# Kernel optimization log

Hardware: AMD Instinct MI355X
Metric: run time of the kernel (lower is better)

Reference implementation:

```python
import jax, jax.numpy as jnp
import numpy as np

N, E = 100000, 1600000
F_IN, H, C = 64, 64, 40


def setup_inputs() -> dict:
    key = jax.random.key(0)
    k = jax.random.split(key, 6)
    x = jax.random.normal(k[0], (N, F_IN), jnp.float32)
    edge_index = jax.random.randint(k[1], (2, E), 0, N, jnp.int32)
    edge_weight = jax.random.uniform(k[2], (E,), jnp.float32)
    W1 = jax.random.normal(k[3], (F_IN, H), jnp.float32) / np.sqrt(F_IN)
    b1 = jnp.zeros((H,), jnp.float32)
    W2 = jax.random.normal(k[4], (H, C), jnp.float32) / np.sqrt(H)
    b2 = jnp.zeros((C,), jnp.float32)
    return {"x": x, "edge_index": edge_index, "edge_weight": edge_weight,
            "W1": W1, "b1": b1, "W2": W2, "b2": b2}


def reference(x, edge_index, edge_weight, W1, b1, W2, b2):
    # PyG GCNConv: add self-loops (weight 1), symmetric normalization
    # D^{-1/2} (A + I) D^{-1/2}, linear transform, scatter-add, bias.
    n = x.shape[0]
    src, dst = edge_index[0], edge_index[1]
    loop = jnp.arange(n, dtype=src.dtype)
    src_f = jnp.concatenate([src, loop])
    dst_f = jnp.concatenate([dst, loop])
    w_f = jnp.concatenate([edge_weight, jnp.ones((n,), edge_weight.dtype)])
    deg = jax.ops.segment_sum(w_f, dst_f, num_segments=n)
    dinv = jnp.where(deg > 0, jax.lax.rsqrt(deg), 0.0)
    norm = dinv[src_f] * w_f * dinv[dst_f]  # [E+N]

    def conv(h, W, b):
        h = h @ W                                    # [n, d_out]
        msg = h[src_f] * norm[:, None]               # gather + scale, [E+N, d_out]
        return jax.ops.segment_sum(msg, dst_f, num_segments=n) + b

    h = jax.nn.relu(conv(x, W1, b1))
    # dropout is identity in eval mode (training=False)
    h = conv(h, W2, b2)
    return jax.nn.log_softmax(h, axis=1)
```

## Files before the change

kernel.cpp:

```cpp
#include <hip/hip_runtime.h>
#include <math.h>

#define N_NODES 100000
#define N_EDGES 1600000
#define C_DIM 40
#define NGROUPS 6250

#define BSZ 256
#define NB  ((N_NODES + BSZ - 1) / BSZ)
#define EB  4096
#define NBE ((N_EDGES + EB - 1) / EB)

#define OFF_DINV 0
#define OFF_BB   100000
#define OFF_CS   100392
#define OFF_ROW  100800
#define OFF_H    200802
#define OFF_REC2 353684
#define OFF_H1P  3553684
#define OFF_H2P  6753684
#define OFF_AGG1 9953684

typedef float floatx4 __attribute__((ext_vector_type(4)));
typedef short shortx8 __attribute__((ext_vector_type(8)));

__device__ inline unsigned short f2bf(float f) {
    unsigned int u = __float_as_uint(f);
    u += 0x7FFF + ((u >> 16) & 1);
    return (unsigned short)(u >> 16);
}
__device__ inline float bf2f(unsigned short h) {
    return __uint_as_float(((unsigned int)h) << 16);
}
__device__ inline float bflo(unsigned int u) { return __uint_as_float(u << 16); }
__device__ inline float bfhi(unsigned int u) { return __uint_as_float(u & 0xFFFF0000u); }

__global__ __launch_bounds__(512) void k_hist2d(const int* __restrict__ ei,
                                                int* __restrict__ H,
                                                int* __restrict__ colsum) {
    __shared__ int bins[NB];
    int t = threadIdx.x, b = blockIdx.x;
    for (int i = t; i < NB; i += 512) bins[i] = 0;
    __syncthreads();
    int base = b * EB;
    for (int i = t; i < EB; i += 512) {
        int e = base + i;
        if (e < N_EDGES) atomicAdd(&bins[ei[N_EDGES + e] >> 8], 1);
    }
    __syncthreads();
    for (int i = t; i < NB; i += 512) {
        int c = bins[i];
        H[b * NB + i] = c;
        if (c) atomicAdd(&colsum[i], c);
    }
}

__global__ __launch_bounds__(512) void k_colscan(int* __restrict__ H,
                                                 const int* __restrict__ colsum,
                                                 int* __restrict__ bucketBase,
                                                 int* __restrict__ rowStart) {
    __shared__ int sd[512];
    __shared__ int sbase;
    int t = threadIdx.x, j = blockIdx.x;
    int p = 0;
    for (int i = t; i < j; i += 512) p += colsum[i];
    sd[t] = p;
    __syncthreads();
    for (int off = 256; off > 0; off >>= 1) {
        if (t < off) sd[t] += sd[t + off];
        __syncthreads();
    }
    if (t == 0) sbase = sd[0];
    __syncthreads();
    int base = sbase;
    if (t == 0) {
        bucketBase[j] = base;
        if (j == NB - 1) { bucketBase[NB] = base + colsum[j]; rowStart[N_NODES] = N_EDGES; }
    }
    __syncthreads();
    int val = (t < NBE) ? H[t * NB + j] : 0;
    sd[t] = val;
    __syncthreads();
    for (int off = 1; off < 512; off <<= 1) {
        int v = (t >= off) ? sd[t - off] : 0;
        __syncthreads();
        sd[t] += v;
        __syncthreads();
    }
    if (t < NBE) H[t * NB + j] = base + sd[t] - val;
}

__global__ __launch_bounds__(512) void k_scatter(const int* __restrict__ ei,
                                                 const float* __restrict__ w,
                                                 const int* __restrict__ blockBase,
                                                 int2* __restrict__ rec) {
    __shared__ int bases[NB];
    __shared__ int cur[NB];
    int t = threadIdx.x, b = blockIdx.x;
    for (int i = t; i < NB; i += 512) { bases[i] = blockBase[b * NB + i]; cur[i] = 0; }
    __syncthreads();
    int base = b * EB;
    for (int i = t; i < EB; i += 512) {
        int e = base + i;
        if (e < N_EDGES) {
            int s = ei[e], d = ei[N_EDGES + e];
            float wv = w[e];
            int bin = d >> 8;
            int pos = bases[bin] + atomicAdd(&cur[bin], 1);
            rec[pos] = make_int2(s | ((d & 255) << 17), __float_as_int(wv));
        }
    }
}

__global__ __launch_bounds__(512) void k_bsort(const int* __restrict__ bucketBase,
                                               const int2* __restrict__ rec,
                                               int2* __restrict__ rec2,
                                               float* __restrict__ dinv,
                                               int* __restrict__ rowStart) {
    __shared__ int   cnt[256];
    __shared__ float wsum[256];
    __shared__ int   cur[256];
    __shared__ int   sd[512];
    int t = threadIdx.x, b = blockIdx.x;
    if (t < 256) { cnt[t] = 0; wsum[t] = 0.f; }
    __syncthreads();
    int r0 = bucketBase[b], r1 = bucketBase[b + 1];
    for (int i = r0 + t; i < r1; i += 512) {
        int2 rv = rec[i];
        int l = (rv.x >> 17) & 255;
        atomicAdd(&cnt[l], 1);
        atomicAdd(&wsum[l], __int_as_float(rv.y));
    }
    __syncthreads();
    int val = (t < 256) ? cnt[t] : 0;
    sd[t] = val;
    __syncthreads();
    for (int off = 1; off < 512; off <<= 1) {
        int v = (t >= off) ? sd[t - off] : 0;
        __syncthreads();
        sd[t] += v;
        __syncthreads();
    }
    float dloc = 0.f;
    if (t < 256) {
        int excl = sd[t] - val;
        cur[t] = excl;
        int node = b * BSZ + t;
        dloc = rsqrtf(1.f + wsum[t]);
        if (node < N_NODES) {
            rowStart[node] = r0 + excl;
            dinv[node] = dloc;
        }
    }
    __syncthreads();
    if (t < 256) wsum[t] = dloc;
    __syncthreads();
    for (int i = r0 + t; i < r1; i += 512) {
        int2 rv = rec[i];
        int l = (rv.x >> 17) & 255;
        float cpart = __int_as_float(rv.y) * wsum[l];
        int pos = r0 + atomicAdd(&cur[l], 1);
        rec2[pos] = make_int2((rv.x & 0x1FFFF) << 7, __float_as_int(cpart));
    }
}

__global__ __launch_bounds__(256) void k_mm1(const float* __restrict__ x,
                                             const float* __restrict__ W1,
                                             const float* __restrict__ dinv,
                                             unsigned short* __restrict__ h1p) {
    int t = threadIdx.x, lane = t & 63, wv = t >> 6;
    int m = lane & 15, quad = lane >> 4;
    int wid = blockIdx.x * 4 + wv, nw = gridDim.x * 4;
    shortx8 B[2][4];
#pragma unroll
    for (int kc = 0; kc < 2; ++kc)
#pragma unroll
        for (int tt = 0; tt < 4; ++tt)
#pragma unroll
            for (int j = 0; j < 8; ++j) {
                int k = kc * 32 + quad * 8 + j;
                B[kc][tt][j] = (short)f2bf(W1[k * 64 + tt * 16 + m]);
            }
    for (int g = wid; g < NGROUPS; g += nw) {
        int n0 = g * 16;
        const float* xr = x + (long)(n0 + m) * 64 + quad * 8;
        floatx4 xa = ((const floatx4*)xr)[0];
        floatx4 xb = ((const floatx4*)(xr + 4))[0];
        floatx4 xc = ((const floatx4*)(xr + 32))[0];
        floatx4 xd = ((const floatx4*)(xr + 36))[0];
        shortx8 A0, A1;
#pragma unroll
        for (int j = 0; j < 4; ++j) {
            A0[j] = (short)f2bf(xa[j]);
            A0[4 + j] = (short)f2bf(xb[j]);
            A1[j] = (short)f2bf(xc[j]);
            A1[4 + j] = (short)f2bf(xd[j]);
        }
        floatx4 acc[4];
#pragma unroll
        for (int tt = 0; tt < 4; ++tt) {
            acc[tt] = (floatx4){0.f, 0.f, 0.f, 0.f};
            acc[tt] = __builtin_amdgcn_mfma_f32_16x16x32_bf16(A0, B[0][tt], acc[tt], 0, 0, 0);
            acc[tt] = __builtin_amdgcn_mfma_f32_16x16x32_bf16(A1, B[1][tt], acc[tt], 0, 0, 0);
        }
        floatx4 dv = ((const floatx4*)(dinv + n0 + quad * 4))[0];
#pragma unroll
        for (int reg = 0; reg < 4; ++reg) {
            int node = n0 + quad * 4 + reg;
            float d = dv[reg];
#pragma unroll
            for (int tt = 0; tt < 4; ++tt)
                h1p[(long)node * 64 + tt * 16 + m] = f2bf(acc[tt][reg] * d);
        }
    }
}

__global__ __launch_bounds__(256) void k_agg1(const int* __restrict__ rowStart,
                                              const int2* __restrict__ rec2,
                                              const float* __restrict__ dinv,
                                              const unsigned short* __restrict__ h1p,
                                              float* __restrict__ agg1) {
    __shared__ int2 cache[4][64];
    int t = threadIdx.x, lane = t & 63, wv = t >> 6;
    int node = blockIdx.x * 4 + wv;
    if (node >= N_NODES) return;
    int2* wc = cache[wv];
    wc[lane] = make_int2(0, 0);
    const char* hb = (const char*)h1p;
    int eslot = lane >> 4;
    int c = lane & 15;
    int lo = c << 3;
    float dn = dinv[node];
    float a0 = 0.f, a1 = 0.f, a2 = 0.f, a3 = 0.f;
    float b0 = 0.f, b1 = 0.f, b2v = 0.f, b3 = 0.f;
    if (eslot == 0) {
        const unsigned int* sp = (const unsigned int*)(hb + ((long)node << 7) + lo);
        unsigned int u0 = sp[0], u1 = sp[1];
        a0 = bflo(u0) * dn; a1 = bfhi(u0) * dn;
        a2 = bflo(u1) * dn; a3 = bfhi(u1) * dn;
    }
    int s0 = rowStart[node], s1 = rowStart[node + 1];
    for (int base = s0; base < s1; base += 64) {
        int idx = base + lane;
        if (idx < s1) wc[lane] = rec2[idx];
        __builtin_amdgcn_wave_barrier();
        int cnt = min(64, s1 - base);
        int j = 0;
        for (; j + 7 < cnt; j += 8) {
            int2 eA = wc[j + eslot];
            int2 eB = wc[j + 4 + eslot];
            const unsigned int* pA = (const unsigned int*)(hb + eA.x + lo);
            const unsigned int* pB = (const unsigned int*)(hb + eB.x + lo);
            unsigned int uA0 = pA[0], uA1 = pA[1];
            unsigned int uB0 = pB[0], uB1 = pB[1];
            float cA = __int_as_float(eA.y), cB = __int_as_float(eB.y);
            a0 = fmaf(bflo(uA0), cA, a0);
            a1 = fmaf(bfhi(uA0), cA, a1);
            a2 = fmaf(bflo(uA1), cA, a2);
            a3 = fmaf(bfhi(uA1), cA, a3);
            b0 = fmaf(bflo(uB0), cB, b0);
            b1 = fmaf(bfhi(uB0), cB, b1);
            b2v = fmaf(bflo(uB1), cB, b2v);
            b3 = fmaf(bfhi(uB1), cB, b3);
        }
        for (; j < cnt; j += 4) {
            int jj = j + eslot;
            bool valid = jj < cnt;
            int2 e = wc[valid ? jj : j];
            float cc = valid ? __int_as_float(e.y) : 0.f;
            const unsigned int* p = (const unsigned int*)(hb + e.x + lo);
            unsigned int u0 = p[0], u1 = p[1];
            a0 = fmaf(bflo(u0), cc, a0);
            a1 = fmaf(bfhi(u0), cc, a1);
            a2 = fmaf(bflo(u1), cc, a2);
            a3 = fmaf(bfhi(u1), cc, a3);
        }
        __builtin_amdgcn_wave_barrier();
    }
    a0 += b0; a1 += b1; a2 += b2v; a3 += b3;
    a0 += __shfl_xor(a0, 16, 64); a0 += __shfl_xor(a0, 32, 64);
    a1 += __shfl_xor(a1, 16, 64); a1 += __shfl_xor(a1, 32, 64);
    a2 += __shfl_xor(a2, 16, 64); a2 += __shfl_xor(a2, 32, 64);
    a3 += __shfl_xor(a3, 16, 64); a3 += __shfl_xor(a3, 32, 64);
    if (eslot == 0) {
        *(float4*)(agg1 + ((long)node << 6) + (c << 2)) = make_float4(a0, a1, a2, a3);
    }
}

__global__ __launch_bounds__(256) void k_mm2(const float* __restrict__ agg1,
                                             const float* __restrict__ b1,
                                             const float* __restrict__ W2,
                                             const float* __restrict__ dinv,
                                             unsigned short* __restrict__ h2p) {
    int t = threadIdx.x, lane = t & 63, wv = t >> 6;
    int m = lane & 15, quad = lane >> 4;
    int wid = blockIdx.x * 4 + wv, nw = gridDim.x * 4;
    shortx8 B[2][3];
#pragma unroll
    for (int kc = 0; kc < 2; ++kc)
#pragma unroll
        for (int tt = 0; tt < 3; ++tt) {
            int n = tt * 16 + m;
#pragma unroll
            for (int j = 0; j < 8; ++j) {
                int k = kc * 32 + quad * 8 + j;
                B[kc][tt][j] = (n < C_DIM) ? (short)f2bf(W2[k * C_DIM + n]) : (short)0;
            }
        }
    floatx4 ba0 = ((const floatx4*)(b1 + quad * 8))[0];
    floatx4 ba1 = ((const floatx4*)(b1 + quad * 8 + 4))[0];
    floatx4 bb0 = ((const floatx4*)(b1 + 32 + quad * 8))[0];
    floatx4 bb1 = ((const floatx4*)(b1 + 32 + quad * 8 + 4))[0];
    for (int g = wid; g < NGROUPS; g += nw) {
        int n0 = g * 16;
        const float* xr = agg1 + (long)(n0 + m) * 64 + quad * 8;
        floatx4 xa = ((const floatx4*)xr)[0];
        floatx4 xb = ((const floatx4*)(xr + 4))[0];
        floatx4 xc = ((const floatx4*)(xr + 32))[0];
        floatx4 xd = ((const floatx4*)(xr + 36))[0];
        shortx8 A0, A1;
#pragma unroll
        for (int j = 0; j < 4; ++j) {
            A0[j]     = (short)f2bf(fmaxf(xa[j] + ba0[j], 0.f));
            A0[4 + j] = (short)f2bf(fmaxf(xb[j] + ba1[j], 0.f));
            A1[j]     = (short)f2bf(fmaxf(xc[j] + bb0[j], 0.f));
            A1[4 + j] = (short)f2bf(fmaxf(xd[j] + bb1[j], 0.f));
        }
        floatx4 acc[3];
#pragma unroll
        for (int tt = 0; tt < 3; ++tt) {
            acc[tt] = (floatx4){0.f, 0.f, 0.f, 0.f};
            acc[tt] = __builtin_amdgcn_mfma_f32_16x16x32_bf16(A0, B[0][tt], acc[tt], 0, 0, 0);
            acc[tt] = __builtin_amdgcn_mfma_f32_16x16x32_bf16(A1, B[1][tt], acc[tt], 0, 0, 0);
        }
        floatx4 dv = ((const floatx4*)(dinv + n0 + quad * 4))[0];
#pragma unroll
        for (int reg = 0; reg < 4; ++reg) {
            int node = n0 + quad * 4 + reg;
            float d = dv[reg];
#pragma unroll
            for (int tt = 0; tt < 3; ++tt) {
                int col = tt * 16 + m;
                if (col < C_DIM)
                    h2p[(long)node * 64 + col] = f2bf(acc[tt][reg] * d);
            }
        }
    }
}

__global__ __launch_bounds__(256) void k_agg2(const int* __restrict__ rowStart,
                                              const int2* __restrict__ rec2,
                                              const float* __restrict__ dinv,
                                              const unsigned short* __restrict__ h2p,
                                              const float* __restrict__ b2,
                                              float* __restrict__ out) {
    __shared__ int2 cache[4][64];
    int t = threadIdx.x, lane = t & 63, wv = t >> 6;
    int node = blockIdx.x * 4 + wv;
    if (node >= N_NODES) return;
    int2* wc = cache[wv];
    wc[lane] = make_int2(0, 0);
    const char* hb = (const char*)h2p;
    int eslot = lane / 20;
    int c = lane - eslot * 20;
    bool elane = eslot < 3;
    int lo = c << 2;
    float dn = dinv[node];
    float alo0 = 0.f, ahi0 = 0.f, alo1 = 0.f, ahi1 = 0.f;
    if (eslot == 0) {
        unsigned int u = *(const unsigned int*)(hb + ((long)node << 7) + lo);
        alo0 = bflo(u) * dn;
        ahi0 = bfhi(u) * dn;
    }
    int s0 = rowStart[node], s1 = rowStart[node + 1];
    for (int base = s0; base < s1; base += 64) {
        int idx = base + lane;
        if (idx < s1) wc[lane] = rec2[idx];
        __builtin_amdgcn_wave_barrier();
        int cnt = min(64, s1 - base);
        int j = 0;
        for (; j + 5 < cnt; j += 6) {
            int2 eA = wc[j + eslot];
            int2 eB = wc[j + 3 + eslot];
            unsigned int uA = *(const unsigned int*)(hb + eA.x + lo);
            unsigned int uB = *(const unsigned int*)(hb + eB.x + lo);
            float cA = elane ? __int_as_float(eA.y) : 0.f;
            float cB = elane ? __int_as_float(eB.y) : 0.f;
            alo0 = fmaf(bflo(uA), cA, alo0);
            ahi0 = fmaf(bfhi(uA), cA, ahi0);
            alo1 = fmaf(bflo(uB), cB, alo1);
            ahi1 = fmaf(bfhi(uB), cB, ahi1);
        }
        for (; j < cnt; j += 3) {
            int jj = j + eslot;
            bool valid = elane && (jj < cnt);
            int2 e = wc[valid ? jj : j];
            float cc = valid ? __int_as_float(e.y) : 0.f;
            unsigned int u = *(const unsigned int*)(hb + e.x + lo);
            alo0 = fmaf(bflo(u), cc, alo0);
            ahi0 = fmaf(bfhi(u), cc, ahi0);
        }
        __builtin_amdgcn_wave_barrier();
    }
    float alo = alo0 + alo1, ahi = ahi0 + ahi1;
    float t1 = __shfl(alo, lane + 20, 64), t2 = __shfl(alo, lane + 40, 64);
    float t3 = __shfl(ahi, lane + 20, 64), t4 = __shfl(ahi, lane + 40, 64);
    alo = alo + t1 + t2;
    ahi = ahi + t3 + t4;
    bool act = lane < 20;
    float2 bb = ((const float2*)b2)[c];
    float vlo = act ? alo + bb.x : -INFINITY;
    float vhi = act ? ahi + bb.y : -INFINITY;
    float m = fmaxf(vlo, vhi);
#pragma unroll
    for (int off = 32; off; off >>= 1) m = fmaxf(m, __shfl_xor(m, off, 64));
    float exlo = act ? expf(vlo - m) : 0.f;
    float exhi = act ? expf(vhi - m) : 0.f;
    float s = exlo + exhi;
#pragma unroll
    for (int off = 32; off; off >>= 1) s += __shfl_xor(s, off, 64);
    float ls = m + logf(s);
    if (act) {
        *(float2*)(out + (long)node * C_DIM + (c << 1)) = make_float2(vlo - ls, vhi - ls);
    }
}

extern "C" void kernel_launch(void* const* d_in, const int* in_sizes, int n_in,
                              void* d_out, int out_size, void* d_ws, size_t ws_size,
                              hipStream_t stream) {
    const float* x  = (const float*)d_in[0];
    const int*   ei = (const int*)d_in[1];
    const float* w  = (const float*)d_in[2];
    const float* W1 = (const float*)d_in[3];
    const float* b1 = (const float*)d_in[4];
    const float* W2 = (const float*)d_in[5];
    const float* b2 = (const float*)d_in[6];
    float* out = (float*)d_out;

    float* wsf = (float*)d_ws;
    int*   wsi = (int*)d_ws;
    float* dinv       = wsf + OFF_DINV;
    int*   bucketBase = wsi + OFF_BB;
    int*   colsum     = wsi + OFF_CS;
    int*   rowStart   = wsi + OFF_ROW;
    int*   H          = wsi + OFF_H;
    int2*  rec2       = (int2*)(wsi + OFF_REC2);
    int2*  rec        = (int2*)(wsi + OFF_H1P);
    unsigned short* h1p = (unsigned short*)(wsi + OFF_H1P);
    unsigned short* h2p = (unsigned short*)(wsi + OFF_H2P);
    float* agg1       = wsf + OFF_AGG1;

    hipMemsetAsync(colsum, 0, NB * sizeof(int), stream);
    k_hist2d<<<NBE, 512, 0, stream>>>(ei, H, colsum);
    k_colscan<<<NB, 512, 0, stream>>>(H, colsum, bucketBase, rowStart);
    k_scatter<<<NBE, 512, 0, stream>>>(ei, w, H, rec);
    k_bsort<<<NB, 512, 0, stream>>>(bucketBase, rec, rec2, dinv, rowStart);

    k_mm1<<<512, 256, 0, stream>>>(x, W1, dinv, h1p);
    k_agg1<<<(N_NODES + 3) / 4, 256, 0, stream>>>(rowStart, rec2, dinv, h1p, agg1);

    k_mm2<<<512, 256, 0, stream>>>(agg1, b1, W2, dinv, h2p);
    k_agg2<<<(N_NODES + 3) / 4, 256, 0, stream>>>(rowStart, rec2, dinv, h2p, b2, out);
}
```

Before: 279.5 us.

## Widen gather loads in aggregation kernels and fuse bias+ReLU+bf16 into agg1

The aggregation kernels now have each lane load 16-byte (agg1) or 8-byte (agg2) chunks of a neighbor row, so more edges are processed per wave iteration with fewer, wider gather instructions. agg1 also applies bias, ReLU and bf16 conversion before writing, so the intermediate is stored as a 64-wide bf16 array instead of fp32. This halves the intermediate traffic between agg1 and mm2 and moves the elementwise work out of mm2. Wider per-lane loads use more registers and spread fewer lanes across each row, which may change occupancy and coalescing.

```diff
diff --git a/kernel.cpp b/kernel.cpp
--- a/kernel.cpp
+++ b/kernel.cpp
@@ -19,7 +19,7 @@
 #define OFF_REC2 353684
 #define OFF_H1P  3553684
 #define OFF_H2P  6753684
-#define OFF_AGG1 9953684
+#define OFF_R1P  9953684
 
 typedef float floatx4 __attribute__((ext_vector_type(4)));
 typedef short shortx8 __attribute__((ext_vector_type(8)));
@@ -219,7 +219,8 @@
                                               const int2* __restrict__ rec2,
                                               const float* __restrict__ dinv,
                                               const unsigned short* __restrict__ h1p,
-                                              float* __restrict__ agg1) {
+                                              const float* __restrict__ b1,
+                                              unsigned short* __restrict__ r1p) {
     __shared__ int2 cache[4][64];
     int t = threadIdx.x, lane = t & 63, wv = t >> 6;
     int node = blockIdx.x * 4 + wv;
@@ -227,17 +228,18 @@
     int2* wc = cache[wv];
     wc[lane] = make_int2(0, 0);
     const char* hb = (const char*)h1p;
-    int eslot = lane >> 4;
-    int c = lane & 15;
-    int lo = c << 3;
+    int eslot = lane >> 3;
+    int c = lane & 7;
+    int lo = c << 4;
     float dn = dinv[node];
-    float a0 = 0.f, a1 = 0.f, a2 = 0.f, a3 = 0.f;
-    float b0 = 0.f, b1 = 0.f, b2v = 0.f, b3 = 0.f;
+    float a0 = 0, a1 = 0, a2 = 0, a3 = 0, a4 = 0, a5 = 0, a6 = 0, a7 = 0;
+    float g0 = 0, g1 = 0, g2 = 0, g3 = 0, g4 = 0, g5 = 0, g6 = 0, g7 = 0;
     if (eslot == 0) {
-        const unsigned int* sp = (const unsigned int*)(hb + ((long)node << 7) + lo);
-        unsigned int u0 = sp[0], u1 = sp[1];
-        a0 = bflo(u0) * dn; a1 = bfhi(u0) * dn;
-        a2 = bflo(u1) * dn; a3 = bfhi(u1) * dn;
+        uint4 u = *(const uint4*)(hb + ((long)node << 7) + lo);
+        a0 = bflo(u.x) * dn; a1 = bfhi(u.x) * dn;
+        a2 = bflo(u.y) * dn; a3 = bfhi(u.y) * dn;
+        a4 = bflo(u.z) * dn; a5 = bfhi(u.z) * dn;
+        a6 = bflo(u.w) * dn; a7 = bfhi(u.w) * dn;
     }
     int s0 = rowStart[node], s1 = rowStart[node + 1];
     for (int base = s0; base < s1; base += 64) {
@@ -246,49 +248,56 @@
         __builtin_amdgcn_wave_barrier();
         int cnt = min(64, s1 - base);
         int j = 0;
-        for (; j + 7 < cnt; j += 8) {
+        for (; j + 15 < cnt; j += 16) {
             int2 eA = wc[j + eslot];
-            int2 eB = wc[j + 4 + eslot];
-            const unsigned int* pA = (const unsigned int*)(hb + eA.x + lo);
-            const unsigned int* pB = (const unsigned int*)(hb + eB.x + lo);
-            unsigned int uA0 = pA[0], uA1 = pA[1];
-            unsigned int uB0 = pB[0], uB1 = pB[1];
+            int2 eB = wc[j + 8 + eslot];
+            uint4 uA = *(const uint4*)(hb + eA.x + lo);
+            uint4 uB = *(const uint4*)(hb + eB.x + lo);
             float cA = __int_as_float(eA.y), cB = __int_as_float(eB.y);
-            a0 = fmaf(bflo(uA0), cA, a0);
-            a1 = fmaf(bfhi(uA0), cA, a1);
-            a2 = fmaf(bflo(uA1), cA, a2);
-            a3 = fmaf(bfhi(uA1), cA, a3);
-            b0 = fmaf(bflo(uB0), cB, b0);
-            b1 = fmaf(bfhi(uB0), cB, b1);
-            b2v = fmaf(bflo(uB1), cB, b2v);
-            b3 = fmaf(bfhi(uB1), cB, b3);
-        }
-        for (; j < cnt; j += 4) {
+            a0 = fmaf(bflo(uA.x), cA, a0); a1 = fmaf(bfhi(uA.x), cA, a1);
+            a2 = fmaf(bflo(uA.y), cA, a2); a3 = fmaf(bfhi(uA.y), cA, a3);
+            a4 = fmaf(bflo(uA.z), cA, a4); a5 = fmaf(bfhi(uA.z), cA, a5);
+            a6 = fmaf(bflo(uA.w), cA, a6); a7 = fmaf(bfhi(uA.w), cA, a7);
+            g0 = fmaf(bflo(uB.x), cB, g0); g1 = fmaf(bfhi(uB.x), cB, g1);
+            g2 = fmaf(bflo(uB.y), cB, g2); g3 = fmaf(bfhi(uB.y), cB, g3);
+            g4 = fmaf(bflo(uB.z), cB, g4); g5 = fmaf(bfhi(uB.z), cB, g5);
+            g6 = fmaf(bflo(uB.w), cB, g6); g7 = fmaf(bfhi(uB.w), cB, g7);
+        }
+        for (; j < cnt; j += 8) {
             int jj = j + eslot;
             bool valid = jj < cnt;
             int2 e = wc[valid ? jj : j];
             float cc = valid ? __int_as_float(e.y) : 0.f;
-            const unsigned int* p = (const unsigned int*)(hb + e.x + lo);
-            unsigned int u0 = p[0], u1 = p[1];
-            a0 = fmaf(bflo(u0), cc, a0);
-            a1 = fmaf(bfhi(u0), cc, a1);
-            a2 = fmaf(bflo(u1), cc, a2);
-            a3 = fmaf(bfhi(u1), cc, a3);
+            uint4 u = *(const uint4*)(hb + e.x + lo);
+            a0 = fmaf(bflo(u.x), cc, a0); a1 = fmaf(bfhi(u.x), cc, a1);
+            a2 = fmaf(bflo(u.y), cc, a2); a3 = fmaf(bfhi(u.y), cc, a3);
+            a4 = fmaf(bflo(u.z), cc, a4); a5 = fmaf(bfhi(u.z), cc, a5);
+            a6 = fmaf(bflo(u.w), cc, a6); a7 = fmaf(bfhi(u.w), cc, a7);
         }
         __builtin_amdgcn_wave_barrier();
     }
-    a0 += b0; a1 += b1; a2 += b2v; a3 += b3;
-    a0 += __shfl_xor(a0, 16, 64); a0 += __shfl_xor(a0, 32, 64);
-    a1 += __shfl_xor(a1, 16, 64); a1 += __shfl_xor(a1, 32, 64);
-    a2 += __shfl_xor(a2, 16, 64); a2 += __shfl_xor(a2, 32, 64);
-    a3 += __shfl_xor(a3, 16, 64); a3 += __shfl_xor(a3, 32, 64);
+    a0 += g0; a1 += g1; a2 += g2; a3 += g3;
+    a4 += g4; a5 += g5; a6 += g6; a7 += g7;
+#define RED(v) v += __shfl_xor(v, 8, 64); v += __shfl_xor(v, 16, 64); v += __shfl_xor(v, 32, 64)
+    RED(a0); RED(a1); RED(a2); RED(a3); RED(a4); RED(a5); RED(a6); RED(a7);
+#undef RED
     if (eslot == 0) {
-        *(float4*)(agg1 + ((long)node << 6) + (c << 2)) = make_float4(a0, a1, a2, a3);
-    }
-}
-
-__global__ __launch_bounds__(256) void k_mm2(const float* __restrict__ agg1,
-                                             const float* __restrict__ b1,
+        floatx4 bva = ((const floatx4*)(b1 + (c << 3)))[0];
+        floatx4 bvb = ((const floatx4*)(b1 + (c << 3) + 4))[0];
+        shortx8 v;
+        v[0] = (short)f2bf(fmaxf(a0 + bva[0], 0.f));
+        v[1] = (short)f2bf(fmaxf(a1 + bva[1], 0.f));
+        v[2] = (short)f2bf(fmaxf(a2 + bva[2], 0.f));
+        v[3] = (short)f2bf(fmaxf(a3 + bva[3], 0.f));
+        v[4] = (short)f2bf(fmaxf(a4 + bvb[0], 0.f));
+        v[5] = (short)f2bf(fmaxf(a5 + bvb[1], 0.f));
+        v[6] = (short)f2bf(fmaxf(a6 + bvb[2], 0.f));
+        v[7] = (short)f2bf(fmaxf(a7 + bvb[3], 0.f));
+        *(shortx8*)(r1p + ((long)node << 6) + (c << 3)) = v;
+    }
+}
+
+__global__ __launch_bounds__(256) void k_mm2(const unsigned short* __restrict__ r1p,
                                              const float* __restrict__ W2,
                                              const float* __restrict__ dinv,
                                              unsigned short* __restrict__ h2p) {
@@ -307,25 +316,11 @@
                 B[kc][tt][j] = (n < C_DIM) ? (short)f2bf(W2[k * C_DIM + n]) : (short)0;
             }
         }
-    floatx4 ba0 = ((const floatx4*)(b1 + quad * 8))[0];
-    floatx4 ba1 = ((const floatx4*)(b1 + quad * 8 + 4))[0];
-    floatx4 bb0 = ((const floatx4*)(b1 + 32 + quad * 8))[0];
-    floatx4 bb1 = ((const floatx4*)(b1 + 32 + quad * 8 + 4))[0];
     for (int g = wid; g < NGROUPS; g += nw) {
         int n0 = g * 16;
-        const float* xr = agg1 + (long)(n0 + m) * 64 + quad * 8;
-        floatx4 xa = ((const floatx4*)xr)[0];
-        floatx4 xb = ((const floatx4*)(xr + 4))[0];
-        floatx4 xc = ((const floatx4*)(xr + 32))[0];
-        floatx4 xd = ((const floatx4*)(xr + 36))[0];
-        shortx8 A0, A1;
-#pragma unroll
-        for (int j = 0; j < 4; ++j) {
-            A0[j]     = (short)f2bf(fmaxf(xa[j] + ba0[j], 0.f));
-            A0[4 + j] = (short)f2bf(fmaxf(xb[j] + ba1[j], 0.f));
-            A1[j]     = (short)f2bf(fmaxf(xc[j] + bb0[j], 0.f));
-            A1[4 + j] = (short)f2bf(fmaxf(xd[j] + bb1[j], 0.f));
-        }
+        const unsigned short* rr = r1p + ((long)(n0 + m) << 6) + quad * 8;
+        shortx8 A0 = *(const shortx8*)rr;
+        shortx8 A1 = *(const shortx8*)(rr + 32);
         floatx4 acc[3];
 #pragma unroll
         for (int tt = 0; tt < 3; ++tt) {
@@ -342,7 +337,7 @@
             for (int tt = 0; tt < 3; ++tt) {
                 int col = tt * 16 + m;
                 if (col < C_DIM)
-                    h2p[(long)node * 64 + col] = f2bf(acc[tt][reg] * d);
+                    h2p[((long)node << 6) + col] = f2bf(acc[tt][reg] * d);
             }
         }
     }
@@ -361,16 +356,17 @@
     int2* wc = cache[wv];
     wc[lane] = make_int2(0, 0);
     const char* hb = (const char*)h2p;
-    int eslot = lane / 20;
-    int c = lane - eslot * 20;
-    bool elane = eslot < 3;
-    int lo = c << 2;
+    int eslot = lane / 10;
+    int c = lane - eslot * 10;
+    bool elane = eslot < 6;
+    int lo = c << 3;
     float dn = dinv[node];
-    float alo0 = 0.f, ahi0 = 0.f, alo1 = 0.f, ahi1 = 0.f;
+    float a0 = 0, a1 = 0, a2 = 0, a3 = 0;
+    float g0 = 0, g1 = 0, g2 = 0, g3 = 0;
     if (eslot == 0) {
-        unsigned int u = *(const unsigned int*)(hb + ((long)node << 7) + lo);
-        alo0 = bflo(u) * dn;
-        ahi0 = bfhi(u) * dn;
+        uint2 u = *(const uint2*)(hb + ((long)node << 7) + lo);
+        a0 = bflo(u.x) * dn; a1 = bfhi(u.x) * dn;
+        a2 = bflo(u.y) * dn; a3 = bfhi(u.y) * dn;
     }
     int s0 = rowStart[node], s1 = rowStart[node + 1];
     for (int base = s0; base < s1; base += 64) {
@@ -379,49 +375,50 @@
         __builtin_amdgcn_wave_barrier();
         int cnt = min(64, s1 - base);
         int j = 0;
-        for (; j + 5 < cnt; j += 6) {
+        for (; j + 11 < cnt; j += 12) {
             int2 eA = wc[j + eslot];
-            int2 eB = wc[j + 3 + eslot];
-            unsigned int uA = *(const unsigned int*)(hb + eA.x + lo);
-            unsigned int uB = *(const unsigned int*)(hb + eB.x + lo);
+            int2 eB = wc[j + 6 + eslot];
+            uint2 uA = *(const uint2*)(hb + eA.x + lo);
+            uint2 uB = *(const uint2*)(hb + eB.x + lo);
             float cA = elane ? __int_as_float(eA.y) : 0.f;
             float cB = elane ? __int_as_float(eB.y) : 0.f;
-            alo0 = fmaf(bflo(uA), cA, alo0);
-            ahi0 = fmaf(bfhi(uA), cA, ahi0);
-            alo1 = fmaf(bflo(uB), cB, alo1);
-            ahi1 = fmaf(bfhi(uB), cB, ahi1);
-        }
-        for (; j < cnt; j += 3) {
+            a0 = fmaf(bflo(uA.x), cA, a0); a1 = fmaf(bfhi(uA.x), cA, a1);
+            a2 = fmaf(bflo(uA.y), cA, a2); a3 = fmaf(bfhi(uA.y), cA, a3);
+            g0 = fmaf(bflo(uB.x), cB, g0); g1 = fmaf(bfhi(uB.x), cB, g1);
+            g2 = fmaf(bflo(uB.y), cB, g2); g3 = fmaf(bfhi(uB.y), cB, g3);
+        }
+        for (; j < cnt; j += 6) {
             int jj = j + eslot;
             bool valid = elane && (jj < cnt);
             int2 e = wc[valid ? jj : j];
             float cc = valid ? __int_as_float(e.y) : 0.f;
-            unsigned int u = *(const unsigned int*)(hb + e.x + lo);
-            alo0 = fmaf(bflo(u), cc, alo0);
-            ahi0 = fmaf(bfhi(u), cc, ahi0);
+            uint2 u = *(const uint2*)(hb + e.x + lo);
+            a0 = fmaf(bflo(u.x), cc, a0); a1 = fmaf(bfhi(u.x), cc, a1);
+            a2 = fmaf(bflo(u.y), cc, a2); a3 = fmaf(bfhi(u.y), cc, a3);
         }
         __builtin_amdgcn_wave_barrier();
     }
-    float alo = alo0 + alo1, ahi = ahi0 + ahi1;
-    float t1 = __shfl(alo, lane + 20, 64), t2 = __shfl(alo, lane + 40, 64);
-    float t3 = __shfl(ahi, lane + 20, 64), t4 = __shfl(ahi, lane + 40, 64);
-    alo = alo + t1 + t2;
-    ahi = ahi + t3 + t4;
-    bool act = lane < 20;
-    float2 bb = ((const float2*)b2)[c];
-    float vlo = act ? alo + bb.x : -INFINITY;
-    float vhi = act ? ahi + bb.y : -INFINITY;
-    float m = fmaxf(vlo, vhi);
+    a0 += g0; a1 += g1; a2 += g2; a3 += g3;
+#define RED6(v) v += __shfl(v, (lane + 30) & 63, 64); \
+                v += __shfl(v, (lane + 10) & 63, 64) + __shfl(v, (lane + 20) & 63, 64)
+    RED6(a0); RED6(a1); RED6(a2); RED6(a3);
+#undef RED6
+    bool act = lane < 10;
+    floatx4 bb = act ? ((const floatx4*)(b2 + (c << 2)))[0] : (floatx4){0, 0, 0, 0};
+    float v0 = act ? a0 + bb[0] : -INFINITY;
+    float v1 = act ? a1 + bb[1] : -INFINITY;
+    float v2 = act ? a2 + bb[2] : -INFINITY;
+    float v3 = act ? a3 + bb[3] : -INFINITY;
+    float m = fmaxf(fmaxf(v0, v1), fmaxf(v2, v3));
 #pragma unroll
     for (int off = 32; off; off >>= 1) m = fmaxf(m, __shfl_xor(m, off, 64));
-    float exlo = act ? expf(vlo - m) : 0.f;
-    float exhi = act ? expf(vhi - m) : 0.f;
-    float s = exlo + exhi;
+    float s = act ? (expf(v0 - m) + expf(v1 - m)) + (expf(v2 - m) + expf(v3 - m)) : 0.f;
 #pragma unroll
     for (int off = 32; off; off >>= 1) s += __shfl_xor(s, off, 64);
     float ls = m + logf(s);
     if (act) {
-        *(float2*)(out + (long)node * C_DIM + (c << 1)) = make_float2(vlo - ls, vhi - ls);
+        *(float4*)(out + (long)node * C_DIM + (c << 2)) =
+            make_float4(v0 - ls, v1 - ls, v2 - ls, v3 - ls);
     }
 }
 
@@ -448,7 +445,7 @@
     int2*  rec        = (int2*)(wsi + OFF_H1P);
     unsigned short* h1p = (unsigned short*)(wsi + OFF_H1P);
     unsigned short* h2p = (unsigned short*)(wsi + OFF_H2P);
-    float* agg1       = wsf + OFF_AGG1;
+    unsigned short* r1p = (unsigned short*)(wsi + OFF_R1P);
 
     hipMemsetAsync(colsum, 0, NB * sizeof(int), stream);
     k_hist2d<<<NBE, 512, 0, stream>>>(ei, H, colsum);
@@ -457,8 +454,8 @@
     k_bsort<<<NB, 512, 0, stream>>>(bucketBase, rec, rec2, dinv, rowStart);
 
     k_mm1<<<512, 256, 0, stream>>>(x, W1, dinv, h1p);
-    k_agg1<<<(N_NODES + 3) / 4, 256, 0, stream>>>(rowStart, rec2, dinv, h1p, agg1);
-
-    k_mm2<<<512, 256, 0, stream>>>(agg1, b1, W2, dinv, h2p);
+    k_agg1<<<(N_NODES + 3) / 4, 256, 0, stream>>>(rowStart, rec2, dinv, h1p, b1, r1p);
+
+    k_mm2<<<512, 256, 0, stream>>>(r1p, W2, dinv, h2p);
     k_agg2<<<(N_NODES + 3) / 4, 256, 0, stream>>>(rowStart, rec2, dinv, h2p, b2, out);
 }
```

Result: no change. 280.4 us (+0.3%).
